# Kernel tuning notes

Measured on AMD Instinct MI355X. Metric: run time of the kernel, lower is better.

## Reference

```python
import math
import jax, jax.numpy as jnp
import numpy as np

B, T, N, D = 8, 12, 512, 64
NN = 16           # neighbors per node
S_FACTOR = 5      # self.s
D_HEAD = 64       # self.d (scaling)
M_SAMPLES = int(S_FACTOR * math.log2(N))  # 45


def _ln(x):
    # LayerNorm over last dim, no affine (elementwise_affine=False)
    mu = jnp.mean(x, axis=-1, keepdims=True)
    var = jnp.var(x, axis=-1, keepdims=True)
    return (x - mu) / jnp.sqrt(var + 1e-5)


def setup_inputs() -> dict:
    key = jax.random.key(0)
    ks = jax.random.split(key, 16)
    w = lambda k, shp: jax.random.normal(k, shp, dtype=jnp.float32) * 0.05
    inp = {
        "x": jax.random.normal(ks[0], (B, T, N, D), dtype=jnp.float32),
        "adj": jax.random.randint(ks[1], (N, NN), 0, N),
        "eigvec": jax.random.normal(ks[2], (D, N, 1), dtype=jnp.float32),
        "eigvalue": jax.random.normal(ks[3], (D,), dtype=jnp.float32),
        "Wq": w(ks[4], (D, D)), "bq": jnp.zeros((D,), jnp.float32),
        "Wk": w(ks[5], (D, D)), "bk": jnp.zeros((D,), jnp.float32),
        "Wv": w(ks[6], (D, D)), "bv": jnp.zeros((D,), jnp.float32),
        "Wo": w(ks[7], (D, D)), "bo": jnp.zeros((D,), jnp.float32),
        "Wp": w(ks[8], (D, 1)), "bp": jnp.zeros((1,), jnp.float32),
        "W1": w(ks[9], (D, D)), "b1": jnp.zeros((D,), jnp.float32),
        "W2": w(ks[10], (D, D)), "b2": jnp.zeros((D,), jnp.float32),
    }
    return inp


def reference(x, adj, eigvec, eigvalue, Wq, bq, Wk, bk, Wv, bv, Wo, bo, Wp, bp, W1, b1, W2, b2):
    # x_ = x + eigvec^T.squeeze(-1) @ diag(eigvalue)  ->  [N,D] broadcast onto [B,T,N,D]
    ev = jnp.squeeze(eigvec, -1).T * eigvalue[None, :]           # [N,D]
    x_ = x + ev
    Q = x_ @ Wq + bq
    K = x_ @ Wk + bk
    V = x_ @ Wv + bv

    # adjacency-gathered GAT sampling
    K_sample = K[:, :, adj, :]                                   # [B,T,N,NN,D]
    V_sample = V[:, :, adj, :]                                   # [B,T,N,NN,D]
    qk = jnp.einsum('btnd,btnkd->btnk', Q, K_sample)             # [B,T,N,NN]
    gat = jnp.einsum('btnk,btnkd->btnd', qk, V_sample)           # [B,T,N,D]
    M = gat @ Wp[:, 0] + bp[0]                                   # [B,T,N]

    # top-k query selection (set is order-invariant downstream)
    _, M_top = jax.lax.top_k(M, M_SAMPLES)                       # [B,T,m]
    Q_red = jnp.take_along_axis(Q, M_top[..., None], axis=2)     # [B,T,m,D]

    scores = jnp.einsum('btmd,btnd->btmn', Q_red, K) / (D_HEAD ** 0.5)
    attn = jax.nn.softmax(scores, axis=-1)                       # [B,T,m,N]

    # argmax-indexed value gather: value[b,t,n] = (attn @ V)[b,t, argmax_m attn[:, n]]
    cp = jnp.argmax(attn, axis=2)                                # [B,T,N]
    av = jnp.einsum('btmn,btnd->btmd', attn, V)                  # [B,T,m,D]
    value = jnp.take_along_axis(av, cp[..., None], axis=2)       # [B,T,N,D]

    value = _ln(value @ Wo + bo + x_)
    h = jax.nn.relu(value @ W1 + b1) @ W2 + b2
    return _ln(h + value)
```

## Files before the change

kernel.cpp:

```cpp
#include <hip/hip_runtime.h>
#include <math.h>

#define Bb 8
#define Tt 12
#define Nn 512
#define Dd 64
#define NNe 16
#define MS 45
#define BT (Bb*Tt)
#define ROWS (BT*Nn)

static __device__ __forceinline__ float bcast_lane(float v, int e) {
    return __uint_as_float(__builtin_amdgcn_readlane(__float_as_uint(v), e));
}
static __device__ __forceinline__ float wave_sum(float v) {
    for (int off = 32; off; off >>= 1) v += __shfl_xor(v, off, 64);
    return v;
}
static __device__ __forceinline__ float wave_max(float v) {
    for (int off = 32; off; off >>= 1) v = fmaxf(v, __shfl_xor(v, off, 64));
    return v;
}

__global__ __launch_bounds__(256) void k_evT(
    const float* __restrict__ eigvec, const float* __restrict__ eigvalue,
    float* __restrict__ evT)
{
    const int i = blockIdx.x * 256 + threadIdx.x;
    const int d = i >> 9, n = i & (Nn - 1);
    evT[n*Dd + d] = eigvec[i] * eigvalue[d];
}

__global__ __launch_bounds__(256) void k_qkv(
    const float* __restrict__ x, const float* __restrict__ evT,
    const float* __restrict__ Wq, const float* __restrict__ bq,
    const float* __restrict__ Wk, const float* __restrict__ bk,
    const float* __restrict__ Wv, const float* __restrict__ bv,
    const float* __restrict__ Wp,
    float* __restrict__ Qo, float* __restrict__ Ko,
    float* __restrict__ Vo, float* __restrict__ pv)
{
    __shared__ __attribute__((aligned(16))) float sWq[Dd*Dd], sWk[Dd*Dd], sWv[Dd*Dd];
    {
        const float4* a = reinterpret_cast<const float4*>(Wq);
        const float4* b = reinterpret_cast<const float4*>(Wk);
        const float4* c = reinterpret_cast<const float4*>(Wv);
        float4* sa = reinterpret_cast<float4*>(sWq);
        float4* sb = reinterpret_cast<float4*>(sWk);
        float4* sc = reinterpret_cast<float4*>(sWv);
        #pragma unroll
        for (int i = 0; i < 4; ++i) {
            sa[i*256 + threadIdx.x] = a[i*256 + threadIdx.x];
            sb[i*256 + threadIdx.x] = b[i*256 + threadIdx.x];
            sc[i*256 + threadIdx.x] = c[i*256 + threadIdx.x];
        }
    }
    __syncthreads();
    const int wave = threadIdx.x >> 6, lane = threadIdx.x & 63;
    const int base = blockIdx.x * 32 + wave * 8;

    float xs[8];
    #pragma unroll
    for (int r = 0; r < 8; ++r) {
        int row = base + r, n = row & (Nn - 1);
        xs[r] = x[(size_t)row*Dd + lane] + evT[n*Dd + lane];
    }
    float q[8], k[8], vv[8];
    #pragma unroll
    for (int r = 0; r < 8; ++r) { q[r] = bq[lane]; k[r] = bk[lane]; vv[r] = bv[lane]; }

    for (int e = 0; e < Dd; ++e) {
        float wq = sWq[e*Dd + lane], wk = sWk[e*Dd + lane], wv = sWv[e*Dd + lane];
        #pragma unroll
        for (int r = 0; r < 8; ++r) {
            float xe = bcast_lane(xs[r], e);
            q[r]  += xe * wq;
            k[r]  += xe * wk;
            vv[r] += xe * wv;
        }
    }
    const float wp = Wp[lane];
    #pragma unroll
    for (int r = 0; r < 8; ++r) {
        size_t off = (size_t)(base + r)*Dd + lane;
        Qo[off] = q[r]; Ko[off] = k[r]; Vo[off] = vv[r];
        float p = wave_sum(vv[r] * wp);
        if (lane == 0) pv[base + r] = p;
    }
}

__global__ __launch_bounds__(256) void k_M(
    const float* __restrict__ Q, const float* __restrict__ K,
    const int* __restrict__ adj, const float* __restrict__ pv,
    const float* __restrict__ bp, float* __restrict__ Mout)
{
    __shared__ __attribute__((aligned(16))) float sK[Nn*Dd];
    const int bt = blockIdx.x >> 1;
    const int half = blockIdx.x & 1;

    const float4* Ksrc = reinterpret_cast<const float4*>(K + (size_t)bt*Nn*Dd);
    float4* sK4 = reinterpret_cast<float4*>(sK);
    for (int i4 = threadIdx.x; i4 < Nn*16; i4 += 256) {
        int nn = i4 >> 4, e4 = i4 & 15;
        sK4[(nn << 4) | (e4 ^ (nn & 15))] = Ksrc[i4];
    }
    __syncthreads();

    const int n = half*256 + threadIdx.x;
    float4 q4[16];
    const float4* Qr = reinterpret_cast<const float4*>(Q + ((size_t)bt*Nn + n)*Dd);
    #pragma unroll
    for (int i = 0; i < 16; ++i) q4[i] = Qr[i];

    const float* pvbt = pv + (size_t)bt*Nn;
    float m = bp[0];
    #pragma unroll 1
    for (int k = 0; k < NNe; ++k) {
        const int j = adj[(n << 4) + k];
        const float4* kr = sK4 + ((size_t)j << 4);
        const int sw = j & 15;
        float dot = 0.f;
        #pragma unroll
        for (int e4 = 0; e4 < 16; ++e4) {
            float4 kv = kr[e4 ^ sw];
            dot += q4[e4].x*kv.x + q4[e4].y*kv.y + q4[e4].z*kv.z + q4[e4].w*kv.w;
        }
        m += dot * pvbt[j];
    }
    Mout[bt*Nn + n] = m;
}

__global__ __launch_bounds__(256) void k_topk(
    const float* __restrict__ Mv, int* __restrict__ Mtop)
{
    const int bt = blockIdx.x * 4 + (threadIdx.x >> 6);
    const int lane = threadIdx.x & 63;
    float v[8];
    #pragma unroll
    for (int i = 0; i < 8; ++i) v[i] = Mv[bt*Nn + i*64 + lane];
    for (int s = 0; s < MS; ++s) {
        float bv = v[0]; int bn = lane;
        #pragma unroll
        for (int i = 1; i < 8; ++i) {
            int nn = i*64 + lane;
            if (v[i] > bv) { bv = v[i]; bn = nn; }
        }
        for (int off = 32; off; off >>= 1) {
            float ov = __shfl_xor(bv, off, 64);
            int   on = __shfl_xor(bn, off, 64);
            if (ov > bv || (ov == bv && on < bn)) { bv = ov; bn = on; }
        }
        if (lane == 0) Mtop[bt*MS + s] = bn;
        const int wl = bn & 63, wi = bn >> 6;
        if (lane == wl) {
            #pragma unroll
            for (int i = 0; i < 8; ++i) if (i == wi) v[i] = -INFINITY;
        }
    }
}

__global__ __launch_bounds__(256) void k_scores(
    const float* __restrict__ Q, const float* __restrict__ K,
    const int* __restrict__ Mtop, float* __restrict__ attn)
{
    __shared__ __attribute__((aligned(16))) float sK[Dd*132];
    __shared__ __attribute__((aligned(16))) float sQ[MS*Dd];
    const int bt = blockIdx.x >> 2;
    const int n0 = (blockIdx.x & 3) * 128;
    const float* Kbt = K + (size_t)bt*Nn*Dd;
    const float* Qbt = Q + (size_t)bt*Nn*Dd;
    for (int i = threadIdx.x; i < 128*Dd; i += 256) {
        int nloc = i >> 6, e = i & 63;
        sK[e*132 + nloc] = Kbt[(n0 + nloc)*Dd + e];
    }
    for (int i = threadIdx.x; i < MS*Dd; i += 256) {
        int m = i >> 6, e = i & 63;
        sQ[i] = Qbt[(size_t)Mtop[bt*MS + m]*Dd + e];
    }
    __syncthreads();
    for (int tile = threadIdx.x; tile < 480; tile += 256) {
        const int m0 = (tile >> 5) * 3;
        const int ng = (tile & 31) * 4;
        float ax[3][4] = {};
        for (int e = 0; e < Dd; ++e) {
            const float4 kv = *reinterpret_cast<const float4*>(&sK[e*132 + ng]);
            #pragma unroll
            for (int i = 0; i < 3; ++i) {
                float qv = sQ[(m0 + i)*Dd + e];
                ax[i][0] += qv * kv.x; ax[i][1] += qv * kv.y;
                ax[i][2] += qv * kv.z; ax[i][3] += qv * kv.w;
            }
        }
        #pragma unroll
        for (int i = 0; i < 3; ++i) {
            float4 o;
            o.x = ax[i][0]*0.125f; o.y = ax[i][1]*0.125f;
            o.z = ax[i][2]*0.125f; o.w = ax[i][3]*0.125f;
            *reinterpret_cast<float4*>(
                &attn[((size_t)bt*MS + m0 + i)*Nn + n0 + ng]) = o;
        }
    }
}

__global__ __launch_bounds__(256) void k_softmax(float* __restrict__ attn)
{
    const int gw = blockIdx.x * 4 + (threadIdx.x >> 6);
    const int lane = threadIdx.x & 63;
    if (gw >= BT*MS) return;
    float* row = attn + (size_t)gw*Nn;
    float v[8];
    float mx = -INFINITY;
    #pragma unroll
    for (int i = 0; i < 8; ++i) { v[i] = row[i*64 + lane]; mx = fmaxf(mx, v[i]); }
    mx = wave_max(mx);
    float sum = 0.f;
    #pragma unroll
    for (int i = 0; i < 8; ++i) { v[i] = expf(v[i] - mx); sum += v[i]; }
    sum = wave_sum(sum);
    float inv = 1.f / sum;
    #pragma unroll
    for (int i = 0; i < 8; ++i) row[i*64 + lane] = v[i] * inv;
}

__global__ __launch_bounds__(256) void k_av(
    const float* __restrict__ attn, const float* __restrict__ V,
    float* __restrict__ av)
{
    const int gw = blockIdx.x * 4 + (threadIdx.x >> 6);
    const int lane = threadIdx.x & 63;
    if (gw >= BT*9) return;
    const int bt = gw / 9, m0 = (gw % 9) * 5;
    const float* a0 = attn + ((size_t)bt*MS + m0)*Nn;
    const float* Vbt = V + (size_t)bt*Nn*Dd;
    float acc[5] = {0,0,0,0,0};
    for (int n = 0; n < Nn; ++n) {
        float v = Vbt[n*Dd + lane];
        #pragma unroll
        for (int i = 0; i < 5; ++i) acc[i] += a0[(size_t)i*Nn + n] * v;
    }
    #pragma unroll
    for (int i = 0; i < 5; ++i)
        av[((size_t)bt*MS + m0 + i)*Dd + lane] = acc[i];
}

__global__ __launch_bounds__(256) void k_cp(
    const float* __restrict__ attn, int* __restrict__ cp)
{
    const int t = blockIdx.x * 256 + threadIdx.x;
    const int bt = t >> 9, n = t & (Nn - 1);
    const float* a = attn + (size_t)bt*MS*Nn + n;
    float best = a[0]; int bi = 0;
    for (int m = 1; m < MS; ++m) {
        float v = a[(size_t)m*Nn];
        if (v > best) { best = v; bi = m; }
    }
    cp[t] = bi;
}

__global__ __launch_bounds__(256) void k_final(
    const float* __restrict__ av, const int* __restrict__ cp,
    const float* __restrict__ x, const float* __restrict__ evT,
    const float* __restrict__ Wo, const float* __restrict__ bo,
    const float* __restrict__ W1, const float* __restrict__ b1,
    const float* __restrict__ W2, const float* __restrict__ b2,
    float* __restrict__ out)
{
    __shared__ __attribute__((aligned(16))) float sW[Dd*Dd];
    const int wave = threadIdx.x >> 6, lane = threadIdx.x & 63;
    const int base = blockIdx.x * 32 + wave * 8;
    const int bt = base >> 9;

    const float4* Wo4 = reinterpret_cast<const float4*>(Wo);
    const float4* W14 = reinterpret_cast<const float4*>(W1);
    const float4* W24 = reinterpret_cast<const float4*>(W2);
    float4* sW4 = reinterpret_cast<float4*>(sW);

    float g[8], o[8];
    #pragma unroll
    for (int r = 0; r < 8; ++r) {
        int row = base + r, n = row & (Nn - 1);
        int c = cp[row];
        g[r] = av[((size_t)bt*MS + c)*Dd + lane];
        o[r] = bo[lane] + x[(size_t)row*Dd + lane] + evT[n*Dd + lane];
    }
    #pragma unroll
    for (int i = 0; i < 4; ++i) sW4[i*256 + threadIdx.x] = Wo4[i*256 + threadIdx.x];
    __syncthreads();

    for (int e = 0; e < Dd; ++e) {
        float w = sW[e*Dd + lane];
        #pragma unroll
        for (int r = 0; r < 8; ++r) o[r] += bcast_lane(g[r], e) * w;
    }
    float val[8];
    #pragma unroll
    for (int r = 0; r < 8; ++r) {
        float mu = wave_sum(o[r]) * (1.f/64.f);
        float d  = o[r] - mu;
        float vs = wave_sum(d*d) * (1.f/64.f);
        val[r] = d * rsqrtf(vs + 1e-5f);
    }
    __syncthreads();
    #pragma unroll
    for (int i = 0; i < 4; ++i) sW4[i*256 + threadIdx.x] = W14[i*256 + threadIdx.x];
    __syncthreads();

    float u[8];
    #pragma unroll
    for (int r = 0; r < 8; ++r) u[r] = b1[lane];
    for (int e = 0; e < Dd; ++e) {
        float w = sW[e*Dd + lane];
        #pragma unroll
        for (int r = 0; r < 8; ++r) u[r] += bcast_lane(val[r], e) * w;
    }
    #pragma unroll
    for (int r = 0; r < 8; ++r) u[r] = fmaxf(u[r], 0.f);
    __syncthreads();
    #pragma unroll
    for (int i = 0; i < 4; ++i) sW4[i*256 + threadIdx.x] = W24[i*256 + threadIdx.x];
    __syncthreads();

    float h[8];
    #pragma unroll
    for (int r = 0; r < 8; ++r) h[r] = b2[lane];
    for (int e = 0; e < Dd; ++e) {
        float w = sW[e*Dd + lane];
        #pragma unroll
        for (int r = 0; r < 8; ++r) h[r] += bcast_lane(u[r], e) * w;
    }
    #pragma unroll
    for (int r = 0; r < 8; ++r) {
        float x2 = h[r] + val[r];
        float mu = wave_sum(x2) * (1.f/64.f);
        float d  = x2 - mu;
        float vs = wave_sum(d*d) * (1.f/64.f);
        out[(size_t)(base + r)*Dd + lane] = d * rsqrtf(vs + 1e-5f);
    }
}

extern "C" void kernel_launch(void* const* d_in, const int* in_sizes, int n_in,
                              void* d_out, int out_size, void* d_ws, size_t ws_size,
                              hipStream_t stream)
{
    const float* x        = (const float*)d_in[0];
    const int*   adj      = (const int*)  d_in[1];
    const float* eigvec   = (const float*)d_in[2];
    const float* eigvalue = (const float*)d_in[3];
    const float* Wq = (const float*)d_in[4],  *bq = (const float*)d_in[5];
    const float* Wk = (const float*)d_in[6],  *bk = (const float*)d_in[7];
    const float* Wv = (const float*)d_in[8],  *bv = (const float*)d_in[9];
    const float* Wo = (const float*)d_in[10], *bo = (const float*)d_in[11];
    const float* Wp = (const float*)d_in[12], *bp = (const float*)d_in[13];
    const float* W1 = (const float*)d_in[14], *b1 = (const float*)d_in[15];
    const float* W2 = (const float*)d_in[16], *b2 = (const float*)d_in[17];

    const size_t RD = (size_t)ROWS * Dd;
    float* ws   = (float*)d_ws;
    float* Q    = ws;
    float* K    = Q + RD;
    float* V    = K + RD;
    float* Mv   = V + RD;
    float* attn = Mv + ROWS;
    float* av   = attn + (size_t)BT*MS*Nn;
    float* pv   = av + (size_t)BT*MS*Dd;
    float* evT  = pv + ROWS;
    int*   Mtop = (int*)(evT + Nn*Dd);
    int*   cp   = Mtop + BT*MS;
    float* out  = (float*)d_out;

    k_evT   <<<(Dd*Nn)/256, 256, 0, stream>>>(eigvec, eigvalue, evT);
    k_qkv   <<<ROWS/32, 256, 0, stream>>>(x, evT, Wq,bq, Wk,bk, Wv,bv, Wp, Q, K, V, pv);
    k_M     <<<BT*2,    256, 0, stream>>>(Q, K, adj, pv, bp, Mv);
    k_topk  <<<BT/4,    256, 0, stream>>>(Mv, Mtop);
    k_scores<<<BT*4,    256, 0, stream>>>(Q, K, Mtop, attn);
    k_softmax<<<(BT*MS)/4, 256, 0, stream>>>(attn);
    k_av    <<<(BT*9)/4, 256, 0, stream>>>(attn, V, av);
    k_cp    <<<ROWS/256, 256, 0, stream>>>(attn, cp);
    k_final <<<ROWS/32, 256, 0, stream>>>(av, cp, x, evT, Wo,bo, W1,b1, W2,b2, out);
}
```

Baseline: 278.6 us.

## Replace in-place softmax with row stats and recompute probabilities in consumers

```diff
diff --git a/kernel.cpp b/kernel.cpp
--- a/kernel.cpp
+++ b/kernel.cpp
@@ -161,7 +161,7 @@
 
 __global__ __launch_bounds__(256) void k_scores(
     const float* __restrict__ Q, const float* __restrict__ K,
-    const int* __restrict__ Mtop, float* __restrict__ attn)
+    const int* __restrict__ Mtop, float* __restrict__ S)
 {
     __shared__ __attribute__((aligned(16))) float sK[Dd*132];
     __shared__ __attribute__((aligned(16))) float sQ[MS*Dd];
@@ -197,17 +197,17 @@
             o.x = ax[i][0]*0.125f; o.y = ax[i][1]*0.125f;
             o.z = ax[i][2]*0.125f; o.w = ax[i][3]*0.125f;
             *reinterpret_cast<float4*>(
-                &attn[((size_t)bt*MS + m0 + i)*Nn + n0 + ng]) = o;
-        }
-    }
-}
-
-__global__ __launch_bounds__(256) void k_softmax(float* __restrict__ attn)
+                &S[((size_t)bt*MS + m0 + i)*Nn + n0 + ng]) = o;
+        }
+    }
+}
+
+__global__ __launch_bounds__(256) void k_stats(
+    const float* __restrict__ S, float2* __restrict__ st)
 {
     const int gw = blockIdx.x * 4 + (threadIdx.x >> 6);
     const int lane = threadIdx.x & 63;
-    if (gw >= BT*MS) return;
-    float* row = attn + (size_t)gw*Nn;
+    const float* row = S + (size_t)gw*Nn;
     float v[8];
     float mx = -INFINITY;
     #pragma unroll
@@ -215,44 +215,58 @@
     mx = wave_max(mx);
     float sum = 0.f;
     #pragma unroll
-    for (int i = 0; i < 8; ++i) { v[i] = expf(v[i] - mx); sum += v[i]; }
+    for (int i = 0; i < 8; ++i) sum += expf(v[i] - mx);
     sum = wave_sum(sum);
-    float inv = 1.f / sum;
-    #pragma unroll
-    for (int i = 0; i < 8; ++i) row[i*64 + lane] = v[i] * inv;
+    if (lane == 0) st[gw] = make_float2(mx, 1.f / sum);
 }
 
 __global__ __launch_bounds__(256) void k_av(
-    const float* __restrict__ attn, const float* __restrict__ V,
-    float* __restrict__ av)
-{
-    const int gw = blockIdx.x * 4 + (threadIdx.x >> 6);
-    const int lane = threadIdx.x & 63;
-    if (gw >= BT*9) return;
-    const int bt = gw / 9, m0 = (gw % 9) * 5;
-    const float* a0 = attn + ((size_t)bt*MS + m0)*Nn;
+    const float* __restrict__ S, const float2* __restrict__ st,
+    const float* __restrict__ V, float* __restrict__ av)
+{
+    __shared__ float sPm[4][5][128];
+    __shared__ float sP[4][5][64];
+    const int bt = blockIdx.x / 9, mg = blockIdx.x % 9, m0 = mg * 5;
+    const int wave = threadIdx.x >> 6, lane = threadIdx.x & 63;
+    const float* Sb = S + ((size_t)bt*MS + m0)*Nn;
+    const float2* stb = st + bt*MS + m0;
     const float* Vbt = V + (size_t)bt*Nn*Dd;
+    const int nb = wave * 128;
+
+    for (int j = lane; j < 5*128; j += 64) {
+        int i = j >> 7, nn = j & 127;
+        float2 sv = stb[i];
+        sPm[wave][i][nn] = expf(Sb[(size_t)i*Nn + nb + nn] - sv.x) * sv.y;
+    }
     float acc[5] = {0,0,0,0,0};
-    for (int n = 0; n < Nn; ++n) {
-        float v = Vbt[n*Dd + lane];
-        #pragma unroll
-        for (int i = 0; i < 5; ++i) acc[i] += a0[(size_t)i*Nn + n] * v;
-    }
-    #pragma unroll
-    for (int i = 0; i < 5; ++i)
-        av[((size_t)bt*MS + m0 + i)*Dd + lane] = acc[i];
+    for (int nn = 0; nn < 128; ++nn) {
+        float v = Vbt[(nb + nn)*Dd + lane];
+        #pragma unroll
+        for (int i = 0; i < 5; ++i) acc[i] += sPm[wave][i][nn] * v;
+    }
+    #pragma unroll
+    for (int i = 0; i < 5; ++i) sP[wave][i][lane] = acc[i];
+    __syncthreads();
+    for (int o = threadIdx.x; o < 5*64; o += 256) {
+        int i = o >> 6, d = o & 63;
+        av[((size_t)bt*MS + m0 + i)*Dd + d] =
+            sP[0][i][d] + sP[1][i][d] + sP[2][i][d] + sP[3][i][d];
+    }
 }
 
 __global__ __launch_bounds__(256) void k_cp(
-    const float* __restrict__ attn, int* __restrict__ cp)
+    const float* __restrict__ S, const float2* __restrict__ st,
+    int* __restrict__ cp)
 {
     const int t = blockIdx.x * 256 + threadIdx.x;
     const int bt = t >> 9, n = t & (Nn - 1);
-    const float* a = attn + (size_t)bt*MS*Nn + n;
-    float best = a[0]; int bi = 0;
-    for (int m = 1; m < MS; ++m) {
-        float v = a[(size_t)m*Nn];
-        if (v > best) { best = v; bi = m; }
+    const float* s = S + (size_t)bt*MS*Nn + n;
+    const float2* stb = st + bt*MS;
+    float best = -INFINITY; int bi = 0;
+    for (int m = 0; m < MS; ++m) {
+        float2 sv = stb[m];
+        float p = expf(s[(size_t)m*Nn] - sv.x) * sv.y;
+        if (p > best) { best = p; bi = m; }
     }
     cp[t] = bi;
 }
@@ -356,25 +370,26 @@
 
     const size_t RD = (size_t)ROWS * Dd;
     float* ws   = (float*)d_ws;
-    float* Q    = ws;
+    float* evT  = ws;
+    float* pv   = evT + (size_t)Nn*Dd;
+    float* Mv   = pv + ROWS;
+    float2* st  = (float2*)(Mv + ROWS);
+    int*   Mtop = (int*)(st + BT*MS);
+    int*   cp   = Mtop + BT*MS;
+    float* av   = (float*)(cp + ROWS);
+    float* Q    = av + (size_t)BT*MS*Dd;
     float* K    = Q + RD;
     float* V    = K + RD;
-    float* Mv   = V + RD;
-    float* attn = Mv + ROWS;
-    float* av   = attn + (size_t)BT*MS*Nn;
-    float* pv   = av + (size_t)BT*MS*Dd;
-    float* evT  = pv + ROWS;
-    int*   Mtop = (int*)(evT + Nn*Dd);
-    int*   cp   = Mtop + BT*MS;
+    float* S    = V + RD;
     float* out  = (float*)d_out;
 
     k_evT   <<<(Dd*Nn)/256, 256, 0, stream>>>(eigvec, eigvalue, evT);
     k_qkv   <<<ROWS/32, 256, 0, stream>>>(x, evT, Wq,bq, Wk,bk, Wv,bv, Wp, Q, K, V, pv);
     k_M     <<<BT*2,    256, 0, stream>>>(Q, K, adj, pv, bp, Mv);
     k_topk  <<<BT/4,    256, 0, stream>>>(Mv, Mtop);
-    k_scores<<<BT*4,    256, 0, stream>>>(Q, K, Mtop, attn);
-    k_softmax<<<(BT*MS)/4, 256, 0, stream>>>(attn);
-    k_av    <<<(BT*9)/4, 256, 0, stream>>>(attn, V, av);
-    k_cp    <<<ROWS/256, 256, 0, stream>>>(attn, cp);
+    k_scores<<<BT*4,    256, 0, stream>>>(Q, K, Mtop, S);
+    k_stats <<<(BT*MS)/4, 256, 0, stream>>>(S, st);
+    k_av    <<<BT*9,    256, 0, stream>>>(S, st, V, av);
+    k_cp    <<<ROWS/256, 256, 0, stream>>>(S, st, cp);
     k_final <<<ROWS/32, 256, 0, stream>>>(av, cp, x, evT, Wo,bo, W1,b1, W2,b2, out);
 }
```

Result: slower. 298.0 us (+6.9%).
